# Kernel tuning notes

Measured on AMD Instinct MI355X. Metric: run time of the kernel, lower is better.

The kernel has to match this reference:

```python
import jax, jax.numpy as jnp
import numpy as np

N_GROUPS, K_POS, HID, M_NEG = 4096, 4, 256, 256


def setup_inputs() -> dict:
    key = jax.random.key(0)
    k1, k2, k3 = jax.random.split(key, 3)
    n, k, h, m = N_GROUPS, K_POS, HID, M_NEG
    embeddings = jax.random.normal(k1, (n * k, h), dtype=jnp.float32)
    # linear_predictor: Linear((k-1)*h -> h)
    W = jax.random.normal(k2, (h, (k - 1) * h), dtype=jnp.float32) / np.float32(np.sqrt((k - 1) * h))
    b = jnp.zeros((h,), dtype=jnp.float32)
    # grouped targets: k consecutive samples share a class id
    target = (jnp.arange(n * k, dtype=jnp.int32) // k).astype(jnp.int32)
    # column index into each group's sorted list of (n-1)*k negatives
    neg_perm = jax.random.randint(k3, (n, m), 0, (n - 1) * k, dtype=jnp.int32)
    return {
        "embeddings": embeddings,
        "W": W,
        "b": b,
        "target": target,
        "neg_perm": neg_perm,
        "k_pos_samples": K_POS,
    }


def reference(embeddings, W, b, target, neg_perm, k_pos_samples):
    # target is implicit in the contiguous group layout (k identical ids per group)
    N, h = embeddings.shape
    k = k_pos_samples
    n = N // k
    m = neg_perm.shape[1]

    e = embeddings.reshape(n, k, h)
    hist_x = e[:, : k - 1, :].reshape(n, (k - 1) * h)   # context: first k-1 of group
    hist_y = e[:, k - 1, :]                              # positive: last of group

    predicts = hist_x @ W.T + b                          # [n, h]
    pos_logit = jnp.sum(predicts * hist_y, axis=-1)      # [n]

    # sorted negatives for group i are {0..i*k-1} u {(i+1)*k..n*k-1};
    # candidate position j maps to global index j (j < i*k) else j + k
    row_off = jnp.arange(n, dtype=neg_perm.dtype)[:, None] * k
    neg_idx = neg_perm + jnp.where(neg_perm >= row_off, k, 0)  # [n, m]

    neg_embed = embeddings[neg_idx]                      # [n, m, h] big gather
    neg_logit = jnp.einsum('nh,nmh->nm', predicts, neg_embed)

    logits = jnp.concatenate([pos_logit[:, None], neg_logit], axis=-1)  # [n, 1+m]
    loss = -jnp.mean(jax.nn.log_softmax(logits, axis=-1)[:, 0])
    return loss
```

## Files before the change

### kernel.cpp

```cpp
#include <hip/hip_runtime.h>

#define N_GROUPS 4096
#define K_POS 4
#define HID 256
#define M_NEG 256
#define KDIM 768
#define N_EMB (N_GROUPS * K_POS)

typedef __attribute__((ext_vector_type(4))) float f32x4;
typedef __attribute__((ext_vector_type(4))) int i32x4;

#define QSCALE 32.0f
#define WSCALE 512.0f
#define QDESCALE (1.0f / (QSCALE * QSCALE))
#define GDESCALE (1.0f / (QSCALE * WSCALE))

__device__ inline ushort f2bf(float f) {
  uint x = __float_as_uint(f);
  return (ushort)((x + 0x7fffu + ((x >> 16) & 1u)) >> 16);
}
__device__ inline float bf2f(ushort u) { return __uint_as_float(((uint)u) << 16); }

__device__ inline int q8(float x, float scale) {
  int q = __float2int_rn(x * scale);
  return max(-127, min(127, q));
}
__device__ inline int pack4(float a, float b, float c, float d, float s) {
  return (q8(a, s) & 0xff) | ((q8(b, s) & 0xff) << 8) |
         ((q8(c, s) & 0xff) << 16) | ((q8(d, s) & 0xff) << 24);
}

#define N4_EMB (N_EMB * HID / 4)
#define N4_W   (KDIM * HID / 4)
__global__ __launch_bounds__(256) void convert_in(
    const float* __restrict__ emb, const float* __restrict__ W,
    int* __restrict__ embQ, int* __restrict__ WQ) {
  const int i = blockIdx.x * 256 + threadIdx.x;
  if (i < N4_EMB) {
    const float4 v = ((const float4*)emb)[i];
    embQ[i] = pack4(v.x, v.y, v.z, v.w, QSCALE);
  } else if (i < N4_EMB + N4_W) {
    const int j = i - N4_EMB;
    const float4 v = ((const float4*)W)[j];
    WQ[j] = pack4(v.x, v.y, v.z, v.w, WSCALE);
  }
}

__global__ __launch_bounds__(256) void gemm_i8(
    const int* __restrict__ embQ, const int* __restrict__ WQ,
    const float* __restrict__ bias, ushort* __restrict__ predB) {
  const int wv = threadIdx.x >> 6, l = threadIdx.x & 63;
  const int mt = blockIdx.x * 4 + wv;
  const int nt = blockIdx.y;
  const int r = l & 15, g = l >> 4;

  const int* A = embQ + (size_t)(mt * 16 + r) * (K_POS * HID / 4) + g * 4;
  const int* B = WQ + (size_t)(nt * 16 + r) * (KDIM / 4) + g * 4;

  i32x4 acc = {0, 0, 0, 0};
#pragma unroll
  for (int kk = 0; kk < 12; ++kk) {
    const i32x4 a = *(const i32x4*)(A + kk * 16);
    const i32x4 b = *(const i32x4*)(B + kk * 16);
    acc = __builtin_amdgcn_mfma_i32_16x16x64_i8(a, b, acc, 0, 0, 0);
  }
  const int col = nt * 16 + r;
  const float bb = bias[col];
#pragma unroll
  for (int i = 0; i < 4; ++i)
    predB[(size_t)(mt * 16 + g * 4 + i) * HID + col] =
        f2bf((float)acc[i] * GDESCALE + bb);
}

__global__ __launch_bounds__(256) void loss_mfma(
    const float* __restrict__ emb, const int* __restrict__ embQ,
    const ushort* __restrict__ predB, const int* __restrict__ neg_perm,
    float* __restrict__ row_loss) {
  const int tid = threadIdx.x;
  const int lane = tid & 63, wv = tid >> 6;
  const int n = blockIdx.x * 2 + (wv >> 1);
  const int half = wv & 1;
  const int jl = lane & 15, g = lane >> 4;
  const int base = n * K_POS;
  __shared__ float smax[4], ssum[4], spos[4];

  const ushort* pr = predB + (size_t)n * HID;
  i32x4 aQ[4];
#pragma unroll
  for (int kk = 0; kk < 4; ++kk) {
    const ushort4 u0 = *(const ushort4*)(pr + kk * 64 + g * 16);
    const ushort4 u1 = *(const ushort4*)(pr + kk * 64 + g * 16 + 4);
    const ushort4 u2 = *(const ushort4*)(pr + kk * 64 + g * 16 + 8);
    const ushort4 u3 = *(const ushort4*)(pr + kk * 64 + g * 16 + 12);
    aQ[kk][0] = pack4(bf2f(u0.x), bf2f(u0.y), bf2f(u0.z), bf2f(u0.w), QSCALE);
    aQ[kk][1] = pack4(bf2f(u1.x), bf2f(u1.y), bf2f(u1.z), bf2f(u1.w), QSCALE);
    aQ[kk][2] = pack4(bf2f(u2.x), bf2f(u2.y), bf2f(u2.z), bf2f(u2.w), QSCALE);
    aQ[kk][3] = pack4(bf2f(u3.x), bf2f(u3.y), bf2f(u3.z), bf2f(u3.w), QSCALE);
  }

  float posv = 0.f;
  if (half == 0) {
    const float4 h = *(const float4*)(emb + ((size_t)n * K_POS + K_POS - 1) * HID + lane * 4);
    const ushort4 p = *(const ushort4*)(pr + lane * 4);
    float s = h.x * bf2f(p.x) + h.y * bf2f(p.y) + h.z * bf2f(p.z) + h.w * bf2f(p.w);
    s += __shfl_xor(s, 1);  s += __shfl_xor(s, 2);  s += __shfl_xor(s, 4);
    s += __shfl_xor(s, 8);  s += __shfl_xor(s, 16); s += __shfl_xor(s, 32);
    posv = s;
  }

  const int* nb = neg_perm + (size_t)n * M_NEG + half * 128;
  int idx[8];
#pragma unroll
  for (int jt = 0; jt < 8; ++jt) {
    const int j = nb[jt * 16 + jl];
    idx[jt] = j + (j >= base ? K_POS : 0);
  }

  float m0 = -INFINITY, s0 = 0.f, m1 = -INFINITY, s1 = 0.f;
#pragma unroll
  for (int t = 0; t < 8; t += 2) {
    const int* bp0 = embQ + (size_t)idx[t] * 64 + g * 4;
    const int* bp1 = embQ + (size_t)idx[t + 1] * 64 + g * 4;
    i32x4 acc0 = {0, 0, 0, 0}, acc1 = {0, 0, 0, 0};
#pragma unroll
    for (int kk = 0; kk < 4; ++kk) {
      const i32x4 b0 = *(const i32x4*)(bp0 + kk * 16);
      acc0 = __builtin_amdgcn_mfma_i32_16x16x64_i8(aQ[kk], b0, acc0, 0, 0, 0);
    }
#pragma unroll
    for (int kk = 0; kk < 4; ++kk) {
      const i32x4 b1 = *(const i32x4*)(bp1 + kk * 16);
      acc1 = __builtin_amdgcn_mfma_i32_16x16x64_i8(aQ[kk], b1, acc1, 0, 0, 0);
    }
    const float v0 = (float)acc0[0] * QDESCALE;
    const float v1 = (float)acc1[0] * QDESCALE;
    { const float mn = fmaxf(m0, v0); s0 = s0 * __expf(m0 - mn) + __expf(v0 - mn); m0 = mn; }
    { const float mn = fmaxf(m1, v1); s1 = s1 * __expf(m1 - mn) + __expf(v1 - mn); m1 = mn; }
  }

  float m = fmaxf(m0, m1);
  float s = s0 * __expf(m0 - m) + s1 * __expf(m1 - m);

  float gm = m;
  gm = fmaxf(gm, __shfl_xor(gm, 1));  gm = fmaxf(gm, __shfl_xor(gm, 2));
  gm = fmaxf(gm, __shfl_xor(gm, 4));  gm = fmaxf(gm, __shfl_xor(gm, 8));
  gm = fmaxf(gm, __shfl_xor(gm, 16)); gm = fmaxf(gm, __shfl_xor(gm, 32));
  float sr = s * __expf(m - gm);
  sr += __shfl_xor(sr, 1);  sr += __shfl_xor(sr, 2);  sr += __shfl_xor(sr, 4);
  sr += __shfl_xor(sr, 8);  sr += __shfl_xor(sr, 16); sr += __shfl_xor(sr, 32);
  sr *= 0.25f;

  if (lane == 0) { smax[wv] = gm; ssum[wv] = sr; spos[wv] = posv; }
  __syncthreads();

  if (half == 0 && lane == 0) {
    const float ma = smax[wv], mb = smax[wv + 1];
    const float sa = ssum[wv], sb = ssum[wv + 1];
    const float pv = spos[wv];
    const float mm = fmaxf(fmaxf(ma, mb), pv);
    const float tot = sa * __expf(ma - mm) + sb * __expf(mb - mm) + __expf(pv - mm);
    row_loss[n] = __logf(tot) + mm - pv;
  }
}

__global__ __launch_bounds__(256) void reduce_mean(
    const float* __restrict__ row_loss, float* __restrict__ out) {
  const int tid = threadIdx.x;
  const int lane = tid & 63, wv = tid >> 6;
  float s = 0.f;
  for (int i = tid; i < N_GROUPS; i += 256) s += row_loss[i];
  s += __shfl_xor(s, 1);  s += __shfl_xor(s, 2);  s += __shfl_xor(s, 4);
  s += __shfl_xor(s, 8);  s += __shfl_xor(s, 16); s += __shfl_xor(s, 32);
  __shared__ float red[4];
  if (lane == 0) red[wv] = s;
  __syncthreads();
  if (tid == 0) out[0] = (red[0] + red[1] + red[2] + red[3]) * (1.0f / N_GROUPS);
}

extern "C" void kernel_launch(void* const* d_in, const int* in_sizes, int n_in,
                              void* d_out, int out_size, void* d_ws, size_t ws_size,
                              hipStream_t stream) {
  const float* emb = (const float*)d_in[0];
  const float* W = (const float*)d_in[1];
  const float* b = (const float*)d_in[2];
  const int* neg_perm = (const int*)d_in[4];
  float* out = (float*)d_out;

  int* embQ = (int*)d_ws;
  int* WQ = embQ + (size_t)N_EMB * HID / 4;
  ushort* predB = (ushort*)(WQ + (size_t)KDIM * HID / 4);
  float* row_loss = (float*)(predB + (size_t)N_GROUPS * HID);

  const int n4 = N4_EMB + N4_W;
  convert_in<<<(n4 + 255) / 256, 256, 0, stream>>>(emb, W, embQ, WQ);
  gemm_i8<<<dim3(N_GROUPS / 64, HID / 16), 256, 0, stream>>>(embQ, WQ, b, predB);
  loss_mfma<<<N_GROUPS / 2, 256, 0, stream>>>(emb, embQ, predB, neg_perm, row_loss);
  reduce_mean<<<1, 256, 0, stream>>>(row_loss, out);
}
```

Baseline: 62.92 us.

## Quantize predictions to int8 inside the GEMM epilogue and reuse A tiles across column tiles

The GEMM now keeps its A fragments in registers and loops over four N tiles per block. It stages results through shared memory and writes predictions directly as packed int8 instead of bf16. The loss kernel loads the prequantized predictions directly and computes the positive logit with an integer dot product against the quantized embeddings, so it no longer reads the fp32 embeddings. The final reduction uses 1024 threads with one float4 per thread. This cuts bf16 conversion work and global traffic, at the cost of extra quantization error in the positive logit.

```diff
diff --git a/kernel.cpp b/kernel.cpp
--- a/kernel.cpp
+++ b/kernel.cpp
@@ -15,12 +15,6 @@
 #define QDESCALE (1.0f / (QSCALE * QSCALE))
 #define GDESCALE (1.0f / (QSCALE * WSCALE))
 
-__device__ inline ushort f2bf(float f) {
-  uint x = __float_as_uint(f);
-  return (ushort)((x + 0x7fffu + ((x >> 16) & 1u)) >> 16);
-}
-__device__ inline float bf2f(ushort u) { return __uint_as_float(((uint)u) << 16); }
-
 __device__ inline int q8(float x, float scale) {
   int q = __float2int_rn(x * scale);
   return max(-127, min(127, q));
@@ -29,6 +23,7 @@
   return (q8(a, s) & 0xff) | ((q8(b, s) & 0xff) << 8) |
          ((q8(c, s) & 0xff) << 16) | ((q8(d, s) & 0xff) << 24);
 }
+__device__ inline int sb(int v, int k) { return (v << (24 - 8 * k)) >> 24; }
 
 #define N4_EMB (N_EMB * HID / 4)
 #define N4_W   (KDIM * HID / 4)
@@ -48,34 +43,42 @@
 
 __global__ __launch_bounds__(256) void gemm_i8(
     const int* __restrict__ embQ, const int* __restrict__ WQ,
-    const float* __restrict__ bias, ushort* __restrict__ predB) {
+    const float* __restrict__ bias, int* __restrict__ predQ) {
   const int wv = threadIdx.x >> 6, l = threadIdx.x & 63;
   const int mt = blockIdx.x * 4 + wv;
-  const int nt = blockIdx.y;
+  const int nt0 = blockIdx.y * 4;
   const int r = l & 15, g = l >> 4;
+  __shared__ float sT[4][16 * 16];
 
   const int* A = embQ + (size_t)(mt * 16 + r) * (K_POS * HID / 4) + g * 4;
-  const int* B = WQ + (size_t)(nt * 16 + r) * (KDIM / 4) + g * 4;
-
-  i32x4 acc = {0, 0, 0, 0};
-#pragma unroll
-  for (int kk = 0; kk < 12; ++kk) {
-    const i32x4 a = *(const i32x4*)(A + kk * 16);
-    const i32x4 b = *(const i32x4*)(B + kk * 16);
-    acc = __builtin_amdgcn_mfma_i32_16x16x64_i8(a, b, acc, 0, 0, 0);
-  }
-  const int col = nt * 16 + r;
-  const float bb = bias[col];
-#pragma unroll
-  for (int i = 0; i < 4; ++i)
-    predB[(size_t)(mt * 16 + g * 4 + i) * HID + col] =
-        f2bf((float)acc[i] * GDESCALE + bb);
+  i32x4 a[12];
+#pragma unroll
+  for (int kk = 0; kk < 12; ++kk) a[kk] = *(const i32x4*)(A + kk * 16);
+
+#pragma unroll
+  for (int j = 0; j < 4; ++j) {
+    const int nt = nt0 + j;
+    const int* B = WQ + (size_t)(nt * 16 + r) * (KDIM / 4) + g * 4;
+    i32x4 acc = {0, 0, 0, 0};
+#pragma unroll
+    for (int kk = 0; kk < 12; ++kk) {
+      const i32x4 b = *(const i32x4*)(B + kk * 16);
+      acc = __builtin_amdgcn_mfma_i32_16x16x64_i8(a[kk], b, acc, 0, 0, 0);
+    }
+    const float bb = bias[nt * 16 + r];
+#pragma unroll
+    for (int i = 0; i < 4; ++i)
+      sT[wv][(g * 4 + i) * 16 + r] = (float)acc[i] * GDESCALE + bb;
+    const int row = l >> 2, cb = l & 3;
+    const float4 v = *(const float4*)&sT[wv][row * 16 + cb * 4];
+    predQ[(size_t)(mt * 16 + row) * (HID / 4) + nt * 4 + cb] =
+        pack4(v.x, v.y, v.z, v.w, QSCALE);
+  }
 }
 
 __global__ __launch_bounds__(256) void loss_mfma(
-    const float* __restrict__ emb, const int* __restrict__ embQ,
-    const ushort* __restrict__ predB, const int* __restrict__ neg_perm,
-    float* __restrict__ row_loss) {
+    const int* __restrict__ embQ, const int* __restrict__ predQ,
+    const int* __restrict__ neg_perm, float* __restrict__ row_loss) {
   const int tid = threadIdx.x;
   const int lane = tid & 63, wv = tid >> 6;
   const int n = blockIdx.x * 2 + (wv >> 1);
@@ -84,28 +87,21 @@
   const int base = n * K_POS;
   __shared__ float smax[4], ssum[4], spos[4];
 
-  const ushort* pr = predB + (size_t)n * HID;
+  const int* pq = predQ + (size_t)n * 64;
   i32x4 aQ[4];
 #pragma unroll
-  for (int kk = 0; kk < 4; ++kk) {
-    const ushort4 u0 = *(const ushort4*)(pr + kk * 64 + g * 16);
-    const ushort4 u1 = *(const ushort4*)(pr + kk * 64 + g * 16 + 4);
-    const ushort4 u2 = *(const ushort4*)(pr + kk * 64 + g * 16 + 8);
-    const ushort4 u3 = *(const ushort4*)(pr + kk * 64 + g * 16 + 12);
-    aQ[kk][0] = pack4(bf2f(u0.x), bf2f(u0.y), bf2f(u0.z), bf2f(u0.w), QSCALE);
-    aQ[kk][1] = pack4(bf2f(u1.x), bf2f(u1.y), bf2f(u1.z), bf2f(u1.w), QSCALE);
-    aQ[kk][2] = pack4(bf2f(u2.x), bf2f(u2.y), bf2f(u2.z), bf2f(u2.w), QSCALE);
-    aQ[kk][3] = pack4(bf2f(u3.x), bf2f(u3.y), bf2f(u3.z), bf2f(u3.w), QSCALE);
-  }
+  for (int kk = 0; kk < 4; ++kk) aQ[kk] = *(const i32x4*)(pq + kk * 16 + g * 4);
 
   float posv = 0.f;
   if (half == 0) {
-    const float4 h = *(const float4*)(emb + ((size_t)n * K_POS + K_POS - 1) * HID + lane * 4);
-    const ushort4 p = *(const ushort4*)(pr + lane * 4);
-    float s = h.x * bf2f(p.x) + h.y * bf2f(p.y) + h.z * bf2f(p.z) + h.w * bf2f(p.w);
+    const int va = pq[lane];
+    const int vb = embQ[(size_t)(base + K_POS - 1) * 64 + lane];
+    int d = sb(va, 0) * sb(vb, 0) + sb(va, 1) * sb(vb, 1) +
+            sb(va, 2) * sb(vb, 2) + sb(va, 3) * sb(vb, 3);
+    float s = (float)d;
     s += __shfl_xor(s, 1);  s += __shfl_xor(s, 2);  s += __shfl_xor(s, 4);
     s += __shfl_xor(s, 8);  s += __shfl_xor(s, 16); s += __shfl_xor(s, 32);
-    posv = s;
+    posv = s * QDESCALE;
   }
 
   const int* nb = neg_perm + (size_t)n * M_NEG + half * 128;
@@ -155,26 +151,31 @@
 
   if (half == 0 && lane == 0) {
     const float ma = smax[wv], mb = smax[wv + 1];
-    const float sa = ssum[wv], sb = ssum[wv + 1];
+    const float sa = ssum[wv], sb2 = ssum[wv + 1];
     const float pv = spos[wv];
     const float mm = fmaxf(fmaxf(ma, mb), pv);
-    const float tot = sa * __expf(ma - mm) + sb * __expf(mb - mm) + __expf(pv - mm);
+    const float tot = sa * __expf(ma - mm) + sb2 * __expf(mb - mm) + __expf(pv - mm);
     row_loss[n] = __logf(tot) + mm - pv;
   }
 }
 
-__global__ __launch_bounds__(256) void reduce_mean(
+__global__ __launch_bounds__(1024) void reduce_mean(
     const float* __restrict__ row_loss, float* __restrict__ out) {
   const int tid = threadIdx.x;
   const int lane = tid & 63, wv = tid >> 6;
-  float s = 0.f;
-  for (int i = tid; i < N_GROUPS; i += 256) s += row_loss[i];
+  const float4 v = ((const float4*)row_loss)[tid];
+  float s = v.x + v.y + v.z + v.w;
   s += __shfl_xor(s, 1);  s += __shfl_xor(s, 2);  s += __shfl_xor(s, 4);
   s += __shfl_xor(s, 8);  s += __shfl_xor(s, 16); s += __shfl_xor(s, 32);
-  __shared__ float red[4];
+  __shared__ float red[16];
   if (lane == 0) red[wv] = s;
   __syncthreads();
-  if (tid == 0) out[0] = (red[0] + red[1] + red[2] + red[3]) * (1.0f / N_GROUPS);
+  if (tid == 0) {
+    float t = 0.f;
+#pragma unroll
+    for (int i = 0; i < 16; ++i) t += red[i];
+    out[0] = t * (1.0f / N_GROUPS);
+  }
 }
 
 extern "C" void kernel_launch(void* const* d_in, const int* in_sizes, int n_in,
@@ -188,12 +189,12 @@
 
   int* embQ = (int*)d_ws;
   int* WQ = embQ + (size_t)N_EMB * HID / 4;
-  ushort* predB = (ushort*)(WQ + (size_t)KDIM * HID / 4);
-  float* row_loss = (float*)(predB + (size_t)N_GROUPS * HID);
+  int* predQ = WQ + (size_t)KDIM * HID / 4;
+  float* row_loss = (float*)(predQ + (size_t)N_GROUPS * HID / 4);
 
   const int n4 = N4_EMB + N4_W;
   convert_in<<<(n4 + 255) / 256, 256, 0, stream>>>(emb, W, embQ, WQ);
-  gemm_i8<<<dim3(N_GROUPS / 64, HID / 16), 256, 0, stream>>>(embQ, WQ, b, predB);
-  loss_mfma<<<N_GROUPS / 2, 256, 0, stream>>>(emb, embQ, predB, neg_perm, row_loss);
-  reduce_mean<<<1, 256, 0, stream>>>(row_loss, out);
-}
+  gemm_i8<<<dim3(N_GROUPS / 64, 4), 256, 0, stream>>>(embQ, WQ, b, predQ);
+  loss_mfma<<<N_GROUPS / 2, 256, 0, stream>>>(embQ, predQ, neg_perm, row_loss);
+  reduce_mean<<<1, 1024, 0, stream>>>(row_loss, out);
+}
```

Result: faster. 55.32 us (-12.1%).
